# Kernel tuning notes

Measured on AMD Instinct MI355X. Metric: run time of the kernel, lower is better.

Reference implementation:

```python
import jax, jax.numpy as jnp
import numpy as np

NEG_FILL = -1e4  # finite stand-in for -inf so sort/cumsum stay NaN-free


def entmax15(X):
    """1.5-entmax along the last axis (Peters et al. 2019, sort-based exact algorithm)."""
    X = X - jnp.max(X, axis=-1, keepdims=True)
    X = X * 0.5  # alpha=1.5 transform
    Xsrt = -jnp.sort(-X, axis=-1)  # descending sort
    S = X.shape[-1]
    rho = jnp.arange(1, S + 1, dtype=X.dtype)  # 1..S support-size candidates
    mean = jnp.cumsum(Xsrt, axis=-1) / rho
    mean_sq = jnp.cumsum(Xsrt * Xsrt, axis=-1) / rho
    ss = rho * (mean_sq - mean * mean)          # running k*variance
    delta = (1.0 - ss) / rho
    tau = mean - jnp.sqrt(jnp.clip(delta, 0.0, None))
    support_size = jnp.sum(tau <= Xsrt, axis=-1, keepdims=True)
    tau_star = jnp.take_along_axis(tau, support_size - 1, axis=-1)
    return jnp.square(jnp.clip(X - tau_star, 0.0, None))


def setup_inputs() -> dict:
    key = jax.random.key(0)
    k1, k2 = jax.random.split(key)
    B, S = 32768, 2048
    scores = jax.random.normal(k1, (B, S), dtype=jnp.float32)
    mask = jax.random.randint(k2, (B, S), 0, 2, dtype=jnp.int32)
    mask = mask.at[:, 0].set(1)  # guarantee at least one unmasked token per row
    return {"scores": scores, "mask": mask}


def reference(scores, mask):
    # replace_masked_values(scores, mask, -inf) -> entmax15(dim=-1)
    masked_scores = jnp.where(mask.astype(bool), scores, NEG_FILL)
    return entmax15(masked_scores)
```

## Files before the change

kernel.cpp:

```cpp
#include <hip/hip_runtime.h>


#define NEG_FILL (-1.0e4f)

typedef float float2v __attribute__((ext_vector_type(2)));
typedef float float4v __attribute__((ext_vector_type(4)));

static constexpr int S_DIM = 2048;
static constexpr int WAVES_PER_BLOCK = 4;
static constexpr int ELEMS = S_DIM / 64;
static constexpr int VEC = ELEMS / 4;
static constexpr int VEC2 = ELEMS / 2;

__global__ __launch_bounds__(256) void entmax15_kernel(
    const float* __restrict__ scores,
    const int*   __restrict__ mask,
    float*       __restrict__ out,
    int nrows)
{
    const int lane = threadIdx.x & 63;
    const int wave = threadIdx.x >> 6;
    const int row  = blockIdx.x * WAVES_PER_BLOCK + wave;
    if (row >= nrows) return;

    const size_t base = (size_t)row * S_DIM;
    const float4* __restrict__ srow = (const float4*)(scores + base);
    const int4*   __restrict__ mrow = (const int4*)(mask + base);
    float4v*      __restrict__ orow = (float4v*)(out + base);

    float x[ELEMS];
    float rmax = -3.402823466e38f;
#pragma unroll
    for (int j = 0; j < VEC; ++j) {
        const float4 s = srow[lane + 64 * j];
        const int4   m = mrow[lane + 64 * j];
        float v0 = m.x ? s.x : NEG_FILL;
        float v1 = m.y ? s.y : NEG_FILL;
        float v2 = m.z ? s.z : NEG_FILL;
        float v3 = m.w ? s.w : NEG_FILL;
        x[4 * j + 0] = v0;
        x[4 * j + 1] = v1;
        x[4 * j + 2] = v2;
        x[4 * j + 3] = v3;
        rmax = fmaxf(rmax, fmaxf(fmaxf(v0, v1), fmaxf(v2, v3)));
    }
#pragma unroll
    for (int off = 32; off >= 1; off >>= 1)
        rmax = fmaxf(rmax, __shfl_xor(rmax, off, 64));

    const float shift = -0.5f * rmax;
    float2v* xv = (float2v*)x;

    const float2v h05  = {0.5f, 0.5f};
    const float2v sh2  = {shift, shift};
    const float2v one2 = {1.0f, 1.0f};
    const float2v zero2 = {0.0f, 0.0f};

    float2v F2 = zero2, G2 = zero2;
    int K = 0;
#pragma unroll
    for (int i = 0; i < VEC2; ++i) {
        float2v t = __builtin_elementwise_fma(xv[i], h05, sh2);
        xv[i] = t;
        float2v d = t + one2;
        float2v y = __builtin_elementwise_max(d, zero2);
        F2 = __builtin_elementwise_fma(y, y, F2);
        G2 = G2 + y;
        K += __popcll(__ballot(d.x > 0.0f));
        K += __popcll(__ballot(d.y > 0.0f));
    }

    float2v FG;
    FG.x = F2.x + F2.y;
    FG.y = G2.x + G2.y;
#pragma unroll
    for (int off = 32; off >= 1; off >>= 1) {
        float2v t;
        t.x = __shfl_xor(FG.x, off, 64);
        t.y = __shfl_xor(FG.y, off, 64);
        FG += t;
    }

    float c     = FG.x - 1.0f;
    float disc  = fmaf(FG.y, FG.y, -(float)K * c);
    float denom = (disc > 0.0f) ? (FG.y + sqrtf(disc)) : (2.0f * FG.y);
    float u     = c / denom;
    float tau   = -1.0f + u;

#pragma unroll 1
    for (int it = 1; it < 16 && fabsf(u) > 2e-7f; ++it) {
        const float2v t2 = {tau, tau};
        F2 = zero2; G2 = zero2; K = 0;
#pragma unroll
        for (int i = 0; i < VEC2; ++i) {
            float2v d = xv[i] - t2;
            float2v y = __builtin_elementwise_max(d, zero2);
            F2 = __builtin_elementwise_fma(y, y, F2);
            G2 = G2 + y;
            K += __popcll(__ballot(d.x > 0.0f));
            K += __popcll(__ballot(d.y > 0.0f));
        }
        FG.x = F2.x + F2.y;
        FG.y = G2.x + G2.y;
#pragma unroll
        for (int off = 32; off >= 1; off >>= 1) {
            float2v t;
            t.x = __shfl_xor(FG.x, off, 64);
            t.y = __shfl_xor(FG.y, off, 64);
            FG += t;
        }
        c     = FG.x - 1.0f;
        disc  = fmaf(FG.y, FG.y, -(float)K * c);
        denom = (disc > 0.0f) ? (FG.y + sqrtf(disc)) : (2.0f * FG.y);
        u     = c / denom;
        tau  += u;
    }

    const float2v t2 = {tau, tau};
#pragma unroll
    for (int j = 0; j < VEC; ++j) {
        float2v ya = __builtin_elementwise_max(xv[2 * j]     - t2, zero2);
        float2v yb = __builtin_elementwise_max(xv[2 * j + 1] - t2, zero2);
        float2v oa = ya * ya;
        float2v ob = yb * yb;
        float4v o;
        o.x = oa.x; o.y = oa.y; o.z = ob.x; o.w = ob.y;
        __builtin_nontemporal_store(o, &orow[lane + 64 * j]);
    }
}

extern "C" void kernel_launch(void* const* d_in, const int* in_sizes, int n_in,
                              void* d_out, int out_size, void* d_ws, size_t ws_size,
                              hipStream_t stream) {
    const float* scores = (const float*)d_in[0];
    const int*   mask   = (const int*)d_in[1];
    float*       out    = (float*)d_out;

    const int nrows = in_sizes[0] / S_DIM;
    const int grid  = (nrows + WAVES_PER_BLOCK - 1) / WAVES_PER_BLOCK;

    entmax15_kernel<<<grid, 256, 0, stream>>>(scores, mask, out, nrows);
}
```

Measured before the change: 598.6 us.

## Process eight rows per wave with register prefetch of next row

Each wave now handles eight consecutive rows instead of one and prefetches the next row's scores and mask into registers while the current row's iterative tau solve runs. The aim is to overlap global loads with the compute-heavy Newton iterations and to cut per-row launch overhead. It also swaps the nontemporal output stores for plain stores. In exchange, the register-held prefetch buffer (64 extra VGPRs per lane) may lower occupancy, and the grid becomes eight times smaller.

```diff
diff --git a/kernel.cpp b/kernel.cpp
--- a/kernel.cpp
+++ b/kernel.cpp
@@ -4,10 +4,10 @@
 #define NEG_FILL (-1.0e4f)
 
 typedef float float2v __attribute__((ext_vector_type(2)));
-typedef float float4v __attribute__((ext_vector_type(4)));
 
 static constexpr int S_DIM = 2048;
 static constexpr int WAVES_PER_BLOCK = 4;
+static constexpr int ROWS_PER_WAVE = 8;
 static constexpr int ELEMS = S_DIM / 64;
 static constexpr int VEC = ELEMS / 4;
 static constexpr int VEC2 = ELEMS / 2;
@@ -20,86 +20,81 @@
 {
     const int lane = threadIdx.x & 63;
     const int wave = threadIdx.x >> 6;
-    const int row  = blockIdx.x * WAVES_PER_BLOCK + wave;
-    if (row >= nrows) return;
+    const int gw   = blockIdx.x * WAVES_PER_BLOCK + wave;
+    const int row0 = gw * ROWS_PER_WAVE;
+    if (row0 >= nrows) return;
 
-    const size_t base = (size_t)row * S_DIM;
-    const float4* __restrict__ srow = (const float4*)(scores + base);
-    const int4*   __restrict__ mrow = (const int4*)(mask + base);
-    float4v*      __restrict__ orow = (float4v*)(out + base);
+    float4 sreg[VEC];
+    int4   mreg[VEC];
 
-    float x[ELEMS];
-    float rmax = -3.402823466e38f;
+    {
+        const float4* __restrict__ s = (const float4*)(scores + (size_t)row0 * S_DIM);
+        const int4*   __restrict__ m = (const int4*)(mask   + (size_t)row0 * S_DIM);
 #pragma unroll
-    for (int j = 0; j < VEC; ++j) {
-        const float4 s = srow[lane + 64 * j];
-        const int4   m = mrow[lane + 64 * j];
-        float v0 = m.x ? s.x : NEG_FILL;
-        float v1 = m.y ? s.y : NEG_FILL;
-        float v2 = m.z ? s.z : NEG_FILL;
-        float v3 = m.w ? s.w : NEG_FILL;
-        x[4 * j + 0] = v0;
-        x[4 * j + 1] = v1;
-        x[4 * j + 2] = v2;
-        x[4 * j + 3] = v3;
-        rmax = fmaxf(rmax, fmaxf(fmaxf(v0, v1), fmaxf(v2, v3)));
+        for (int j = 0; j < VEC; ++j) {
+            sreg[j] = s[lane + 64 * j];
+            mreg[j] = m[lane + 64 * j];
+        }
     }
-#pragma unroll
-    for (int off = 32; off >= 1; off >>= 1)
-        rmax = fmaxf(rmax, __shfl_xor(rmax, off, 64));
 
-    const float shift = -0.5f * rmax;
-    float2v* xv = (float2v*)x;
-
-    const float2v h05  = {0.5f, 0.5f};
-    const float2v sh2  = {shift, shift};
-    const float2v one2 = {1.0f, 1.0f};
+    const float2v h05   = {0.5f, 0.5f};
+    const float2v one2  = {1.0f, 1.0f};
     const float2v zero2 = {0.0f, 0.0f};
 
-    float2v F2 = zero2, G2 = zero2;
-    int K = 0;
+#pragma unroll 1
+    for (int r = 0; r < ROWS_PER_WAVE; ++r) {
+        const int row = row0 + r;
+        if (row >= nrows) break;
+
+        float x[ELEMS];
+        float rmax = -3.402823466e38f;
 #pragma unroll
-    for (int i = 0; i < VEC2; ++i) {
-        float2v t = __builtin_elementwise_fma(xv[i], h05, sh2);
-        xv[i] = t;
-        float2v d = t + one2;
-        float2v y = __builtin_elementwise_max(d, zero2);
-        F2 = __builtin_elementwise_fma(y, y, F2);
-        G2 = G2 + y;
-        K += __popcll(__ballot(d.x > 0.0f));
-        K += __popcll(__ballot(d.y > 0.0f));
-    }
+        for (int j = 0; j < VEC; ++j) {
+            const float4 s = sreg[j];
+            const int4   m = mreg[j];
+            float v0 = m.x ? s.x : NEG_FILL;
+            float v1 = m.y ? s.y : NEG_FILL;
+            float v2 = m.z ? s.z : NEG_FILL;
+            float v3 = m.w ? s.w : NEG_FILL;
+            x[4 * j + 0] = v0;
+            x[4 * j + 1] = v1;
+            x[4 * j + 2] = v2;
+            x[4 * j + 3] = v3;
+            rmax = fmaxf(rmax, fmaxf(fmaxf(v0, v1), fmaxf(v2, v3)));
+        }
 
-    float2v FG;
-    FG.x = F2.x + F2.y;
-    FG.y = G2.x + G2.y;
+        if (r + 1 < ROWS_PER_WAVE && row + 1 < nrows) {
+            const float4* __restrict__ sn = (const float4*)(scores + (size_t)(row + 1) * S_DIM);
+            const int4*   __restrict__ mn = (const int4*)(mask   + (size_t)(row + 1) * S_DIM);
 #pragma unroll
-    for (int off = 32; off >= 1; off >>= 1) {
-        float2v t;
-        t.x = __shfl_xor(FG.x, off, 64);
-        t.y = __shfl_xor(FG.y, off, 64);
-        FG += t;
-    }
+            for (int j = 0; j < VEC; ++j) {
+                sreg[j] = sn[lane + 64 * j];
+                mreg[j] = mn[lane + 64 * j];
+            }
+        }
 
-    float c     = FG.x - 1.0f;
-    float disc  = fmaf(FG.y, FG.y, -(float)K * c);
-    float denom = (disc > 0.0f) ? (FG.y + sqrtf(disc)) : (2.0f * FG.y);
-    float u     = c / denom;
-    float tau   = -1.0f + u;
+#pragma unroll
+        for (int off = 32; off >= 1; off >>= 1)
+            rmax = fmaxf(rmax, __shfl_xor(rmax, off, 64));
 
-#pragma unroll 1
-    for (int it = 1; it < 16 && fabsf(u) > 2e-7f; ++it) {
-        const float2v t2 = {tau, tau};
-        F2 = zero2; G2 = zero2; K = 0;
+        const float2v sh2 = {-0.5f * rmax, -0.5f * rmax};
+        float2v* xv = (float2v*)x;
+
+        float2v F2 = zero2, G2 = zero2;
+        int K = 0;
 #pragma unroll
         for (int i = 0; i < VEC2; ++i) {
-            float2v d = xv[i] - t2;
+            float2v t = __builtin_elementwise_fma(xv[i], h05, sh2);
+            xv[i] = t;
+            float2v d = t + one2;
             float2v y = __builtin_elementwise_max(d, zero2);
             F2 = __builtin_elementwise_fma(y, y, F2);
             G2 = G2 + y;
             K += __popcll(__ballot(d.x > 0.0f));
             K += __popcll(__ballot(d.y > 0.0f));
         }
+
+        float2v FG;
         FG.x = F2.x + F2.y;
         FG.y = G2.x + G2.y;
 #pragma unroll
@@ -109,23 +104,54 @@
             t.y = __shfl_xor(FG.y, off, 64);
             FG += t;
         }
-        c     = FG.x - 1.0f;
-        disc  = fmaf(FG.y, FG.y, -(float)K * c);
-        denom = (disc > 0.0f) ? (FG.y + sqrtf(disc)) : (2.0f * FG.y);
-        u     = c / denom;
-        tau  += u;
-    }
 
-    const float2v t2 = {tau, tau};
+        float c     = FG.x - 1.0f;
+        float disc  = fmaf(FG.y, FG.y, -(float)K * c);
+        float denom = (disc > 0.0f) ? (FG.y + sqrtf(disc)) : (2.0f * FG.y);
+        float u     = c / denom;
+        float tau   = -1.0f + u;
+
+#pragma unroll 1
+        for (int it = 1; it < 16 && fabsf(u) > 2e-7f; ++it) {
+            const float2v t2 = {tau, tau};
+            F2 = zero2; G2 = zero2; K = 0;
 #pragma unroll
-    for (int j = 0; j < VEC; ++j) {
-        float2v ya = __builtin_elementwise_max(xv[2 * j]     - t2, zero2);
-        float2v yb = __builtin_elementwise_max(xv[2 * j + 1] - t2, zero2);
-        float2v oa = ya * ya;
-        float2v ob = yb * yb;
-        float4v o;
-        o.x = oa.x; o.y = oa.y; o.z = ob.x; o.w = ob.y;
-        __builtin_nontemporal_store(o, &orow[lane + 64 * j]);
+            for (int i = 0; i < VEC2; ++i) {
+                float2v d = xv[i] - t2;
+                float2v y = __builtin_elementwise_max(d, zero2);
+                F2 = __builtin_elementwise_fma(y, y, F2);
+                G2 = G2 + y;
+                K += __popcll(__ballot(d.x > 0.0f));
+                K += __popcll(__ballot(d.y > 0.0f));
+            }
+            FG.x = F2.x + F2.y;
+            FG.y = G2.x + G2.y;
+#pragma unroll
+            for (int off = 32; off >= 1; off >>= 1) {
+                float2v t;
+                t.x = __shfl_xor(FG.x, off, 64);
+                t.y = __shfl_xor(FG.y, off, 64);
+                FG += t;
+            }
+            c     = FG.x - 1.0f;
+            disc  = fmaf(FG.y, FG.y, -(float)K * c);
+            denom = (disc > 0.0f) ? (FG.y + sqrtf(disc)) : (2.0f * FG.y);
+            u     = c / denom;
+            tau  += u;
+        }
+
+        float4* __restrict__ orow = (float4*)(out + (size_t)row * S_DIM);
+        const float2v t2 = {tau, tau};
+#pragma unroll
+        for (int j = 0; j < VEC; ++j) {
+            float2v y0 = __builtin_elementwise_max(xv[2 * j]     - t2, zero2);
+            float2v y1 = __builtin_elementwise_max(xv[2 * j + 1] - t2, zero2);
+            float2v o0 = y0 * y0;
+            float2v o1 = y1 * y1;
+            float4 o;
+            o.x = o0.x; o.y = o0.y; o.z = o1.x; o.w = o1.y;
+            orow[lane + 64 * j] = o;
+        }
     }
 }
 
@@ -137,7 +163,8 @@
     float*       out    = (float*)d_out;
 
     const int nrows = in_sizes[0] / S_DIM;
-    const int grid  = (nrows + WAVES_PER_BLOCK - 1) / WAVES_PER_BLOCK;
+    const int rows_per_block = WAVES_PER_BLOCK * ROWS_PER_WAVE;
+    const int grid = (nrows + rows_per_block - 1) / rows_per_block;
 
     entmax15_kernel<<<grid, 256, 0, stream>>>(scores, mask, out, nrows);
 }
```

After: 604.4 us. Within noise of the previous version (+1.0%).

## Process each row with a full block and add support-size early exit

Applied to the files above, without the earlier changes.

Each row is now handled by a 256-thread block with 8 elements per thread instead of one wave holding 32 elements per lane. Per-iteration sums go through LDS with double-buffered slots and block barriers. This cuts register pressure and should raise occupancy, at the cost of an extra barrier per Newton iteration. The iteration now also stops when the support size K stops changing or the step falls below a looser threshold, and the output stores become ordinary rather than nontemporal.

```diff
diff --git a/kernel.cpp b/kernel.cpp
--- a/kernel.cpp
+++ b/kernel.cpp
@@ -1,75 +1,80 @@
 #include <hip/hip_runtime.h>
+#include <stdint.h>
 
 
 #define NEG_FILL (-1.0e4f)
 
 typedef float float2v __attribute__((ext_vector_type(2)));
-typedef float float4v __attribute__((ext_vector_type(4)));
 
-static constexpr int S_DIM = 2048;
-static constexpr int WAVES_PER_BLOCK = 4;
-static constexpr int ELEMS = S_DIM / 64;
-static constexpr int VEC = ELEMS / 4;
-static constexpr int VEC2 = ELEMS / 2;
+static constexpr int S_DIM   = 2048;
+static constexpr int THREADS = 256;
+static constexpr int NWAVES  = THREADS / 64;
+static constexpr int EPT     = S_DIM / THREADS;
+static constexpr int V2      = EPT / 2;
 
-__global__ __launch_bounds__(256) void entmax15_kernel(
+__global__ __launch_bounds__(THREADS) void entmax15_kernel(
     const float* __restrict__ scores,
     const int*   __restrict__ mask,
     float*       __restrict__ out,
     int nrows)
 {
-    const int lane = threadIdx.x & 63;
-    const int wave = threadIdx.x >> 6;
-    const int row  = blockIdx.x * WAVES_PER_BLOCK + wave;
+    __shared__ float red[2][NWAVES][4];
+
+    const int tid  = threadIdx.x;
+    const int lane = tid & 63;
+    const int wv   = tid >> 6;
+    const int row  = blockIdx.x;
     if (row >= nrows) return;
 
     const size_t base = (size_t)row * S_DIM;
     const float4* __restrict__ srow = (const float4*)(scores + base);
     const int4*   __restrict__ mrow = (const int4*)(mask + base);
-    float4v*      __restrict__ orow = (float4v*)(out + base);
+    float4*       __restrict__ orow = (float4*)(out + base);
 
-    float x[ELEMS];
-    float rmax = -3.402823466e38f;
-#pragma unroll
-    for (int j = 0; j < VEC; ++j) {
-        const float4 s = srow[lane + 64 * j];
-        const int4   m = mrow[lane + 64 * j];
-        float v0 = m.x ? s.x : NEG_FILL;
-        float v1 = m.y ? s.y : NEG_FILL;
-        float v2 = m.z ? s.z : NEG_FILL;
-        float v3 = m.w ? s.w : NEG_FILL;
-        x[4 * j + 0] = v0;
-        x[4 * j + 1] = v1;
-        x[4 * j + 2] = v2;
-        x[4 * j + 3] = v3;
-        rmax = fmaxf(rmax, fmaxf(fmaxf(v0, v1), fmaxf(v2, v3)));
-    }
+    const float4 sa = srow[tid];
+    const float4 sb = srow[tid + THREADS];
+    const int4   ma = mrow[tid];
+    const int4   mb = mrow[tid + THREADS];
+
+    float x[EPT];
+    x[0] = ma.x ? sa.x : NEG_FILL;
+    x[1] = ma.y ? sa.y : NEG_FILL;
+    x[2] = ma.z ? sa.z : NEG_FILL;
+    x[3] = ma.w ? sa.w : NEG_FILL;
+    x[4] = mb.x ? sb.x : NEG_FILL;
+    x[5] = mb.y ? sb.y : NEG_FILL;
+    x[6] = mb.z ? sb.z : NEG_FILL;
+    x[7] = mb.w ? sb.w : NEG_FILL;
+
+    float rmax = fmaxf(fmaxf(fmaxf(x[0], x[1]), fmaxf(x[2], x[3])),
+                       fmaxf(fmaxf(x[4], x[5]), fmaxf(x[6], x[7])));
 #pragma unroll
     for (int off = 32; off >= 1; off >>= 1)
         rmax = fmaxf(rmax, __shfl_xor(rmax, off, 64));
+    if (lane == 0) red[0][wv][0] = rmax;
+    __syncthreads();
+    rmax = fmaxf(fmaxf(red[0][0][0], red[0][1][0]),
+                 fmaxf(red[0][2][0], red[0][3][0]));
 
-    const float shift = -0.5f * rmax;
+    const float2v h05   = {0.5f, 0.5f};
+    const float2v one2  = {1.0f, 1.0f};
+    const float2v zero2 = {0.0f, 0.0f};
+    const float2v sh2   = {-0.5f * rmax, -0.5f * rmax};
     float2v* xv = (float2v*)x;
 
-    const float2v h05  = {0.5f, 0.5f};
-    const float2v sh2  = {shift, shift};
-    const float2v one2 = {1.0f, 1.0f};
-    const float2v zero2 = {0.0f, 0.0f};
-
     float2v F2 = zero2, G2 = zero2;
-    int K = 0;
+    int Kw = 0;
 #pragma unroll
-    for (int i = 0; i < VEC2; ++i) {
+    for (int i = 0; i < V2; ++i) {
         float2v t = __builtin_elementwise_fma(xv[i], h05, sh2);
         xv[i] = t;
         float2v d = t + one2;
         float2v y = __builtin_elementwise_max(d, zero2);
         F2 = __builtin_elementwise_fma(y, y, F2);
         G2 = G2 + y;
-        K += __popcll(__ballot(d.x > 0.0f));
-        K += __popcll(__ballot(d.y > 0.0f));
+        Kw += __popcll(__ballot(d.x > 0.0f));
+        Kw += __popcll(__ballot(d.y > 0.0f));
     }
-
     float2v FG;
     FG.x = F2.x + F2.y;
     FG.y = G2.x + G2.y;
@@ -80,25 +85,36 @@
         t.y = __shfl_xor(FG.y, off, 64);
         FG += t;
     }
+    if (lane == 0) {
+        red[1][wv][0] = FG.x;
+        red[1][wv][1] = FG.y;
+        red[1][wv][2] = (float)Kw;
+    }
+    __syncthreads();
+    float F  = red[1][0][0] + red[1][1][0] + red[1][2][0] + red[1][3][0];
+    float G  = red[1][0][1] + red[1][1][1] + red[1][2][1] + red[1][3][1];
+    float Kf = red[1][0][2] + red[1][1][2] + red[1][2][2] + red[1][3][2];
+    int   K  = (int)Kf;
 
-    float c     = FG.x - 1.0f;
-    float disc  = fmaf(FG.y, FG.y, -(float)K * c);
-    float denom = (disc > 0.0f) ? (FG.y + sqrtf(disc)) : (2.0f * FG.y);
+    float c     = F - 1.0f;
+    float disc  = fmaf(G, G, -Kf * c);
+    float denom = (disc > 0.0f) ? (G + sqrtf(disc)) : (2.0f * G);
     float u     = c / denom;
     float tau   = -1.0f + u;
+    int   Kprev = K;
 
 #pragma unroll 1
-    for (int it = 1; it < 16 && fabsf(u) > 2e-7f; ++it) {
+    for (int it = 1; it < 16; ++it) {
         const float2v t2 = {tau, tau};
-        F2 = zero2; G2 = zero2; K = 0;
+        F2 = zero2; G2 = zero2; Kw = 0;
 #pragma unroll
-        for (int i = 0; i < VEC2; ++i) {
+        for (int i = 0; i < V2; ++i) {
             float2v d = xv[i] - t2;
             float2v y = __builtin_elementwise_max(d, zero2);
             F2 = __builtin_elementwise_fma(y, y, F2);
             G2 = G2 + y;
-            K += __popcll(__ballot(d.x > 0.0f));
-            K += __popcll(__ballot(d.y > 0.0f));
+            Kw += __popcll(__ballot(d.x > 0.0f));
+            Kw += __popcll(__ballot(d.y > 0.0f));
         }
         FG.x = F2.x + F2.y;
         FG.y = G2.x + G2.y;
@@ -109,24 +125,41 @@
             t.y = __shfl_xor(FG.y, off, 64);
             FG += t;
         }
-        c     = FG.x - 1.0f;
-        disc  = fmaf(FG.y, FG.y, -(float)K * c);
-        denom = (disc > 0.0f) ? (FG.y + sqrtf(disc)) : (2.0f * FG.y);
+        const int slot = (it & 1) ^ 1;
+        if (lane == 0) {
+            red[slot][wv][0] = FG.x;
+            red[slot][wv][1] = FG.y;
+            red[slot][wv][2] = (float)Kw;
+        }
+        __syncthreads();
+        F  = red[slot][0][0] + red[slot][1][0] + red[slot][2][0] + red[slot][3][0];
+        G  = red[slot][0][1] + red[slot][1][1] + red[slot][2][1] + red[slot][3][1];
+        Kf = red[slot][0][2] + red[slot][1][2] + red[slot][2][2] + red[slot][3][2];
+        K  = (int)Kf;
+
+        c     = F - 1.0f;
+        disc  = fmaf(G, G, -Kf * c);
+        denom = (disc > 0.0f) ? (G + sqrtf(disc)) : (2.0f * G);
         u     = c / denom;
         tau  += u;
+        if (K == Kprev || !(fabsf(u) > 1e-6f)) break;
+        Kprev = K;
     }
 
     const float2v t2 = {tau, tau};
-#pragma unroll
-    for (int j = 0; j < VEC; ++j) {
-        float2v ya = __builtin_elementwise_max(xv[2 * j]     - t2, zero2);
-        float2v yb = __builtin_elementwise_max(xv[2 * j + 1] - t2, zero2);
-        float2v oa = ya * ya;
-        float2v ob = yb * yb;
-        float4v o;
-        o.x = oa.x; o.y = oa.y; o.z = ob.x; o.w = ob.y;
-        __builtin_nontemporal_store(o, &orow[lane + 64 * j]);
-    }
+    float2v o0 = __builtin_elementwise_max(xv[0] - t2, zero2);
+    float2v o1 = __builtin_elementwise_max(xv[1] - t2, zero2);
+    float2v o2 = __builtin_elementwise_max(xv[2] - t2, zero2);
+    float2v o3 = __builtin_elementwise_max(xv[3] - t2, zero2);
+    o0 = o0 * o0;
+    o1 = o1 * o1;
+    o2 = o2 * o2;
+    o3 = o3 * o3;
+    float4 oa, ob;
+    oa.x = o0.x; oa.y = o0.y; oa.z = o1.x; oa.w = o1.y;
+    ob.x = o2.x; ob.y = o2.y; ob.z = o3.x; ob.w = o3.y;
+    orow[tid]           = oa;
+    orow[tid + THREADS] = ob;
 }
 
 extern "C" void kernel_launch(void* const* d_in, const int* in_sizes, int n_in,
@@ -137,7 +170,5 @@
     float*       out    = (float*)d_out;
 
     const int nrows = in_sizes[0] / S_DIM;
-    const int grid  = (nrows + WAVES_PER_BLOCK - 1) / WAVES_PER_BLOCK;
-
-    entmax15_kernel<<<grid, 256, 0, stream>>>(scores, mask, out, nrows);
+    entmax15_kernel<<<nrows, THREADS, 0, stream>>>(scores, mask, out, nrows);
 }
```

After: 593.9 us. Within noise of the previous version (-0.8%).
